# Optimization experiments

Hardware: AMD Instinct MI355X
Metric: run time of the kernel (lower is better)

## Reference

```python
import jax, jax.numpy as jnp
import numpy as np

IS_NORMAL = True
IS_SDF = False
WHITE_BACK = False


def setup_inputs() -> dict:
    key = jax.random.key(0)
    k1, k2, k3, k4 = jax.random.split(key, 4)
    B, R, S, C = 4, 16384, 64, 32
    colors = jax.random.uniform(k1, (B, R, S, C), dtype=jnp.float32)
    densities = jax.random.normal(k2, (B, R, S, 1), dtype=jnp.float32)
    depths = jax.random.uniform(k3, (B, R, S, 1), dtype=jnp.float32)
    grads = jax.random.normal(k4, (B, R, S, 3), dtype=jnp.float32)
    return {"colors": colors, "densities": densities, "depths": depths, "grads": grads}


def reference(colors, densities, depths, grads):
    # midpoint averaging along the sample axis (axis=2)
    deltas = depths[:, :, 1:] - depths[:, :, :-1]            # [B,R,S-1,1]
    colors_mid = (colors[:, :, :-1] + colors[:, :, 1:]) * 0.5
    densities_mid = (densities[:, :, :-1] + densities[:, :, 1:]) * 0.5
    depths_mid = (depths[:, :, :-1] + depths[:, :, 1:]) * 0.5
    grads_mid = (grads[:, :, :-1] + grads[:, :, 1:]) * 0.5

    if not IS_SDF:
        densities_mid = jax.nn.softplus(densities_mid - 1.0)

    density_delta = densities_mid * deltas
    alpha = 1.0 - jnp.exp(-density_delta)                     # [B,R,S-1,1]

    # transmittance via exclusive cumprod of (1 - alpha + 1e-10)
    alpha_shifted = jnp.concatenate(
        [jnp.ones_like(alpha[:, :, :1]), 1.0 - alpha + 1e-10], axis=2)
    weights = alpha * jnp.cumprod(alpha_shifted, axis=2)[:, :, :-1]

    composite_rgb = jnp.sum(weights * colors_mid, axis=2)     # [B,R,C]
    weight_total = jnp.sum(weights, axis=2)                   # [B,R,1]
    composite_depth = jnp.sum(weights * depths_mid, axis=2) / weight_total
    composite_depth = jnp.where(jnp.isnan(composite_depth), jnp.inf, composite_depth)
    composite_depth = jnp.clip(composite_depth, jnp.min(depths), jnp.max(depths))

    composite_grad = jnp.sum(weights * grads_mid, axis=2) + 1.0 - weight_total  # [B,R,3]

    if WHITE_BACK:
        composite_rgb = composite_rgb.at[..., :3].add(1.0 - weight_total)

    composite_rgb = composite_rgb * 2.0 - 1.0
    return (composite_rgb, composite_depth, weights, composite_grad)
```

## Files before the change

kernel.cpp:

```cpp
#include <hip/hip_runtime.h>
#include <math.h>

typedef float fvec4 __attribute__((ext_vector_type(4)));

template <int CTRL, int RM, int BM>
static __device__ __forceinline__ float updf(float oldv, float src) {
  return __int_as_float(__builtin_amdgcn_update_dpp(
      __float_as_int(oldv), __float_as_int(src), CTRL, RM, BM, false));
}

static __device__ __forceinline__ float mul_scan64(float x) {
  x *= updf<0x111, 0xf, 0xf>(1.0f, x);
  x *= updf<0x112, 0xf, 0xf>(1.0f, x);
  x *= updf<0x114, 0xf, 0xe>(1.0f, x);
  x *= updf<0x118, 0xf, 0xc>(1.0f, x);
  x *= updf<0x142, 0xa, 0xf>(1.0f, x);
  x *= updf<0x143, 0xc, 0xf>(1.0f, x);
  return x;
}
static __device__ __forceinline__ float sum64_lane63(float x) {
  x += updf<0x111, 0xf, 0xf>(0.0f, x);
  x += updf<0x112, 0xf, 0xf>(0.0f, x);
  x += updf<0x114, 0xf, 0xe>(0.0f, x);
  x += updf<0x118, 0xf, 0xc>(0.0f, x);
  x += updf<0x142, 0xa, 0xf>(0.0f, x);
  x += updf<0x143, 0xc, 0xf>(0.0f, x);
  return x;
}
static __device__ __forceinline__ float readlane63(float x) {
  return __int_as_float(__builtin_amdgcn_readlane(__float_as_int(x), 63));
}

__global__ __launch_bounds__(256) void minmax_kernel(const float4* __restrict__ d,
                                                     float* __restrict__ ws, int n4) {
  __shared__ float smin[4], smax[4];
  int idx = blockIdx.x * 256 + threadIdx.x;
  int stride = gridDim.x * 256;
  float lmin = INFINITY, lmax = -INFINITY;
  for (int i = idx; i < n4; i += stride) {
    float4 v = d[i];
    lmin = fminf(lmin, fminf(fminf(v.x, v.y), fminf(v.z, v.w)));
    lmax = fmaxf(lmax, fmaxf(fmaxf(v.x, v.y), fmaxf(v.z, v.w)));
  }
#pragma unroll
  for (int off = 32; off; off >>= 1) {
    lmin = fminf(lmin, __shfl_xor(lmin, off));
    lmax = fmaxf(lmax, __shfl_xor(lmax, off));
  }
  const int wid = threadIdx.x >> 6;
  if ((threadIdx.x & 63) == 0) { smin[wid] = lmin; smax[wid] = lmax; }
  __syncthreads();
  if (threadIdx.x == 0) {
    ws[blockIdx.x]       = fminf(fminf(smin[0], smin[1]), fminf(smin[2], smin[3]));
    ws[512 + blockIdx.x] = fmaxf(fmaxf(smax[0], smax[1]), fmaxf(smax[2], smax[3]));
  }
}

__global__ __launch_bounds__(256) void march_lite(
    const float* __restrict__ dens, const float* __restrict__ depths,
    const float* __restrict__ grads, float* __restrict__ out,
    float* __restrict__ coef_ws, const float* __restrict__ mm_part,
    size_t o_depth, size_t o_w, size_t o_grad)
{
  __shared__ float smin[4], smax[4];
  const int lane = threadIdx.x & 63;
  const int wid  = threadIdx.x >> 6;
  const size_t ray = (size_t)blockIdx.x * 4 + wid;

  const float d   = depths[ray * 64 + lane];
  const float den = __builtin_nontemporal_load(dens + ray * 64 + lane);
  const float* gp = grads + ray * 192 + (size_t)lane * 3;
  const float g0 = __builtin_nontemporal_load(gp + 0);
  const float g1 = __builtin_nontemporal_load(gp + 1);
  const float g2 = __builtin_nontemporal_load(gp + 2);

  const float dn    = __shfl_down(d, 1);
  const float denn  = __shfl_down(den, 1);
  const float delta = dn - d;
  const float dm    = 0.5f * (den + denn) - 1.0f;
  const float sp    = fmaxf(dm, 0.0f) + log1pf(expf(-fabsf(dm)));
  const float dd    = sp * delta;
  const float alpha = 1.0f - expf(-dd);
  const float t     = (1.0f - alpha) + 1e-10f;

  const float p = mul_scan64(t);
  float excl = __shfl_up(p, 1);
  if (lane == 0) excl = 1.0f;
  const float w = (lane < 63) ? alpha * excl : 0.0f;

  if (lane < 63)
    __builtin_nontemporal_store(w, out + o_w + ray * 63 + lane);

  float wprev = __shfl_up(w, 1);
  if (lane == 0) wprev = 0.0f;
  const float coef = 0.5f * (w + wprev);
  coef_ws[ray * 64 + lane] = coef;

  const float wt = readlane63(sum64_lane63(w));
  const float s1 = readlane63(sum64_lane63(coef * d));
  const float s2 = readlane63(sum64_lane63(coef * g0));
  const float s3 = readlane63(sum64_lane63(coef * g1));
  const float s4 = readlane63(sum64_lane63(coef * g2));

  {
    float m0 = fminf(mm_part[threadIdx.x], mm_part[threadIdx.x + 256]);
    float m1 = fmaxf(mm_part[512 + threadIdx.x], mm_part[512 + threadIdx.x + 256]);
#pragma unroll
    for (int off = 32; off; off >>= 1) {
      m0 = fminf(m0, __shfl_xor(m0, off));
      m1 = fmaxf(m1, __shfl_xor(m1, off));
    }
    if (lane == 0) { smin[wid] = m0; smax[wid] = m1; }
  }
  __syncthreads();

  if (lane == 0) {
    const float dmin = fminf(fminf(smin[0], smin[1]), fminf(smin[2], smin[3]));
    const float dmax = fmaxf(fmaxf(smax[0], smax[1]), fmaxf(smax[2], smax[3]));
    float cd = s1 / wt;
    if (cd != cd) cd = INFINITY;
    cd = fminf(fmaxf(cd, dmin), dmax);
    out[o_depth + ray] = cd;
    const float add = 1.0f - wt;
    float* og = out + o_grad + ray * 3;
    og[0] = s2 + add;
    og[1] = s3 + add;
    og[2] = s4 + add;
  }
}

__global__ __launch_bounds__(256) void rgb_kernel(
    const float* __restrict__ colors, const float* __restrict__ coef_ws,
    float* __restrict__ out)
{
  const int lane = threadIdx.x & 63;
  const size_t ray = (size_t)blockIdx.x * 4 + (threadIdx.x >> 6);

  const float coef = coef_ws[ray * 64 + lane];

  const fvec4* cp = (const fvec4*)(colors + ray * 2048);
  fvec4 col[8];
#pragma unroll
  for (int k = 0; k < 8; ++k)
    col[k] = __builtin_nontemporal_load(cp + (size_t)k * 64 + lane);

  float a0 = 0.f, a1 = 0.f, a2 = 0.f, a3 = 0.f;
  const int sbase = lane >> 3;
#pragma unroll
  for (int k = 0; k < 8; ++k) {
    const float cf = __shfl(coef, k * 8 + sbase);
    a0 = fmaf(cf, col[k].x, a0);
    a1 = fmaf(cf, col[k].y, a1);
    a2 = fmaf(cf, col[k].z, a2);
    a3 = fmaf(cf, col[k].w, a3);
  }
  a0 += updf<0x128, 0xf, 0xf>(0.0f, a0);
  a1 += updf<0x128, 0xf, 0xf>(0.0f, a1);
  a2 += updf<0x128, 0xf, 0xf>(0.0f, a2);
  a3 += updf<0x128, 0xf, 0xf>(0.0f, a3);
#pragma unroll
  for (int off = 16; off <= 32; off <<= 1) {
    a0 += __shfl_xor(a0, off);
    a1 += __shfl_xor(a1, off);
    a2 += __shfl_xor(a2, off);
    a3 += __shfl_xor(a3, off);
  }
  if (lane < 8) {
    float4 o;
    o.x = fmaf(a0, 2.0f, -1.0f);
    o.y = fmaf(a1, 2.0f, -1.0f);
    o.z = fmaf(a2, 2.0f, -1.0f);
    o.w = fmaf(a3, 2.0f, -1.0f);
    ((float4*)(out + ray * 32))[lane] = o;
  }
}

extern "C" void kernel_launch(void* const* d_in, const int* in_sizes, int n_in,
                              void* d_out, int out_size, void* d_ws, size_t ws_size,
                              hipStream_t stream) {
  const float* colors = (const float*)d_in[0];
  const float* dens   = (const float*)d_in[1];
  const float* depths = (const float*)d_in[2];
  const float* grads  = (const float*)d_in[3];
  float* out = (float*)d_out;
  float* ws  = (float*)d_ws;
  float* coef_ws = ws + 1024;

  const int ndep  = in_sizes[2];
  const int nrays = ndep / 64;
  const int C     = in_sizes[0] / ndep;

  const size_t o_depth = (size_t)nrays * C;
  const size_t o_w     = o_depth + (size_t)nrays;
  const size_t o_grad  = o_w + (size_t)nrays * 63;

  hipLaunchKernelGGL(minmax_kernel, dim3(512), dim3(256), 0, stream,
                     (const float4*)depths, ws, ndep / 4);
  hipLaunchKernelGGL(march_lite, dim3(nrays / 4), dim3(256), 0, stream,
                     dens, depths, grads, out, coef_ws, ws, o_depth, o_w, o_grad);
  hipLaunchKernelGGL(rgb_kernel, dim3(nrays / 4), dim3(256), 0, stream,
                     colors, coef_ws, out);
}
```

Baseline: 129.7 us.

## Fuse march and RGB kernels, fold depth min/max into main pass

Merges the march and RGB compositing kernels into one kernel where each wave processes four rays and keeps the blending coefficients in registers, removing the coef workspace round trip. The separate min/max pass over depths is removed; per-block min/max is computed from depths already loaded, then reduced by a single-block kernel, and a small final kernel applies the clamp to the stored unclamped depths. This avoids re-reading depths and the coef buffer, at the cost of two extra small launches, one of them a serial single-block reduction.

```diff
diff --git a/kernel.cpp b/kernel.cpp
--- a/kernel.cpp
+++ b/kernel.cpp
@@ -31,148 +31,155 @@
   return __int_as_float(__builtin_amdgcn_readlane(__float_as_int(x), 63));
 }
 
-__global__ __launch_bounds__(256) void minmax_kernel(const float4* __restrict__ d,
-                                                     float* __restrict__ ws, int n4) {
-  __shared__ float smin[4], smax[4];
-  int idx = blockIdx.x * 256 + threadIdx.x;
-  int stride = gridDim.x * 256;
-  float lmin = INFINITY, lmax = -INFINITY;
-  for (int i = idx; i < n4; i += stride) {
-    float4 v = d[i];
-    lmin = fminf(lmin, fminf(fminf(v.x, v.y), fminf(v.z, v.w)));
-    lmax = fmaxf(lmax, fmaxf(fmaxf(v.x, v.y), fmaxf(v.z, v.w)));
-  }
-#pragma unroll
-  for (int off = 32; off; off >>= 1) {
-    lmin = fminf(lmin, __shfl_xor(lmin, off));
-    lmax = fmaxf(lmax, __shfl_xor(lmax, off));
-  }
-  const int wid = threadIdx.x >> 6;
-  if ((threadIdx.x & 63) == 0) { smin[wid] = lmin; smax[wid] = lmax; }
-  __syncthreads();
-  if (threadIdx.x == 0) {
-    ws[blockIdx.x]       = fminf(fminf(smin[0], smin[1]), fminf(smin[2], smin[3]));
-    ws[512 + blockIdx.x] = fmaxf(fmaxf(smax[0], smax[1]), fmaxf(smax[2], smax[3]));
-  }
-}
-
-__global__ __launch_bounds__(256) void march_lite(
-    const float* __restrict__ dens, const float* __restrict__ depths,
-    const float* __restrict__ grads, float* __restrict__ out,
-    float* __restrict__ coef_ws, const float* __restrict__ mm_part,
-    size_t o_depth, size_t o_w, size_t o_grad)
+
+__global__ __launch_bounds__(256) void fused_kernel(
+    const float* __restrict__ colors, const float* __restrict__ dens,
+    const float* __restrict__ depths, const float* __restrict__ grads,
+    float* __restrict__ out, float* __restrict__ ws, float* __restrict__ cd_ws,
+    size_t o_w, size_t o_grad, int nb)
 {
   __shared__ float smin[4], smax[4];
   const int lane = threadIdx.x & 63;
   const int wid  = threadIdx.x >> 6;
-  const size_t ray = (size_t)blockIdx.x * 4 + wid;
-
-  const float d   = depths[ray * 64 + lane];
-  const float den = __builtin_nontemporal_load(dens + ray * 64 + lane);
-  const float* gp = grads + ray * 192 + (size_t)lane * 3;
-  const float g0 = __builtin_nontemporal_load(gp + 0);
-  const float g1 = __builtin_nontemporal_load(gp + 1);
-  const float g2 = __builtin_nontemporal_load(gp + 2);
-
-  const float dn    = __shfl_down(d, 1);
-  const float denn  = __shfl_down(den, 1);
-  const float delta = dn - d;
-  const float dm    = 0.5f * (den + denn) - 1.0f;
-  const float sp    = fmaxf(dm, 0.0f) + log1pf(expf(-fabsf(dm)));
-  const float dd    = sp * delta;
-  const float alpha = 1.0f - expf(-dd);
-  const float t     = (1.0f - alpha) + 1e-10f;
-
-  const float p = mul_scan64(t);
-  float excl = __shfl_up(p, 1);
-  if (lane == 0) excl = 1.0f;
-  const float w = (lane < 63) ? alpha * excl : 0.0f;
-
-  if (lane < 63)
-    __builtin_nontemporal_store(w, out + o_w + ray * 63 + lane);
-
-  float wprev = __shfl_up(w, 1);
-  if (lane == 0) wprev = 0.0f;
-  const float coef = 0.5f * (w + wprev);
-  coef_ws[ray * 64 + lane] = coef;
-
-  const float wt = readlane63(sum64_lane63(w));
-  const float s1 = readlane63(sum64_lane63(coef * d));
-  const float s2 = readlane63(sum64_lane63(coef * g0));
-  const float s3 = readlane63(sum64_lane63(coef * g1));
-  const float s4 = readlane63(sum64_lane63(coef * g2));
-
-  {
-    float m0 = fminf(mm_part[threadIdx.x], mm_part[threadIdx.x + 256]);
-    float m1 = fmaxf(mm_part[512 + threadIdx.x], mm_part[512 + threadIdx.x + 256]);
-#pragma unroll
-    for (int off = 32; off; off >>= 1) {
-      m0 = fminf(m0, __shfl_xor(m0, off));
-      m1 = fmaxf(m1, __shfl_xor(m1, off));
-    }
-    if (lane == 0) { smin[wid] = m0; smax[wid] = m1; }
-  }
+  const size_t ray0 = (size_t)blockIdx.x * 16 + (size_t)wid * 4;
+
+  float cf[4];
+  float dmin_w = INFINITY, dmax_w = -INFINITY;
+
+#pragma unroll
+  for (int r = 0; r < 4; ++r) {
+    const size_t ray = ray0 + r;
+    const float d   = depths[ray * 64 + lane];
+    const float den = __builtin_nontemporal_load(dens + ray * 64 + lane);
+    const float* gp = grads + ray * 192 + (size_t)lane * 3;
+    const float g0 = __builtin_nontemporal_load(gp + 0);
+    const float g1 = __builtin_nontemporal_load(gp + 1);
+    const float g2 = __builtin_nontemporal_load(gp + 2);
+
+    dmin_w = fminf(dmin_w, d);
+    dmax_w = fmaxf(dmax_w, d);
+
+    const float dn    = __shfl_down(d, 1);
+    const float denn  = __shfl_down(den, 1);
+    const float delta = dn - d;
+    const float dm    = 0.5f * (den + denn) - 1.0f;
+    const float sp    = fmaxf(dm, 0.0f) + log1pf(expf(-fabsf(dm)));
+    const float dd    = sp * delta;
+    const float alpha = 1.0f - expf(-dd);
+    const float t     = (1.0f - alpha) + 1e-10f;
+
+    const float p = mul_scan64(t);
+    float excl = __shfl_up(p, 1);
+    if (lane == 0) excl = 1.0f;
+    const float w = (lane < 63) ? alpha * excl : 0.0f;
+
+    if (lane < 63)
+      __builtin_nontemporal_store(w, out + o_w + ray * 63 + lane);
+
+    float wprev = __shfl_up(w, 1);
+    if (lane == 0) wprev = 0.0f;
+    const float coef = 0.5f * (w + wprev);
+    cf[r] = coef;
+
+    const float wt = readlane63(sum64_lane63(w));
+    const float s1 = readlane63(sum64_lane63(coef * d));
+    const float s2 = readlane63(sum64_lane63(coef * g0));
+    const float s3 = readlane63(sum64_lane63(coef * g1));
+    const float s4 = readlane63(sum64_lane63(coef * g2));
+
+    if (lane == 0) {
+      float cd = s1 / wt;
+      if (cd != cd) cd = INFINITY;
+      cd_ws[ray] = cd;
+      const float add = 1.0f - wt;
+      float* og = out + o_grad + ray * 3;
+      og[0] = s2 + add;
+      og[1] = s3 + add;
+      og[2] = s4 + add;
+    }
+  }
+
+#pragma unroll
+  for (int off = 32; off; off >>= 1) {
+    dmin_w = fminf(dmin_w, __shfl_xor(dmin_w, off));
+    dmax_w = fmaxf(dmax_w, __shfl_xor(dmax_w, off));
+  }
+  if (lane == 0) { smin[wid] = dmin_w; smax[wid] = dmax_w; }
   __syncthreads();
-
-  if (lane == 0) {
-    const float dmin = fminf(fminf(smin[0], smin[1]), fminf(smin[2], smin[3]));
-    const float dmax = fmaxf(fmaxf(smax[0], smax[1]), fmaxf(smax[2], smax[3]));
-    float cd = s1 / wt;
-    if (cd != cd) cd = INFINITY;
-    cd = fminf(fmaxf(cd, dmin), dmax);
-    out[o_depth + ray] = cd;
-    const float add = 1.0f - wt;
-    float* og = out + o_grad + ray * 3;
-    og[0] = s2 + add;
-    og[1] = s3 + add;
-    og[2] = s4 + add;
-  }
-}
-
-__global__ __launch_bounds__(256) void rgb_kernel(
-    const float* __restrict__ colors, const float* __restrict__ coef_ws,
-    float* __restrict__ out)
+  if (threadIdx.x == 0) {
+    ws[blockIdx.x]      = fminf(fminf(smin[0], smin[1]), fminf(smin[2], smin[3]));
+    ws[nb + blockIdx.x] = fmaxf(fmaxf(smax[0], smax[1]), fmaxf(smax[2], smax[3]));
+  }
+
+  const int sbase = lane >> 3;
+#pragma unroll
+  for (int r = 0; r < 4; ++r) {
+    const size_t ray = ray0 + r;
+    const fvec4* cp = (const fvec4*)(colors + ray * 2048);
+    fvec4 col[8];
+#pragma unroll
+    for (int k = 0; k < 8; ++k)
+      col[k] = __builtin_nontemporal_load(cp + (size_t)k * 64 + lane);
+
+    float a0 = 0.f, a1 = 0.f, a2 = 0.f, a3 = 0.f;
+#pragma unroll
+    for (int k = 0; k < 8; ++k) {
+      const float cfb = __shfl(cf[r], k * 8 + sbase);
+      a0 = fmaf(cfb, col[k].x, a0);
+      a1 = fmaf(cfb, col[k].y, a1);
+      a2 = fmaf(cfb, col[k].z, a2);
+      a3 = fmaf(cfb, col[k].w, a3);
+    }
+    a0 += updf<0x128, 0xf, 0xf>(0.0f, a0);
+    a1 += updf<0x128, 0xf, 0xf>(0.0f, a1);
+    a2 += updf<0x128, 0xf, 0xf>(0.0f, a2);
+    a3 += updf<0x128, 0xf, 0xf>(0.0f, a3);
+#pragma unroll
+    for (int off = 16; off <= 32; off <<= 1) {
+      a0 += __shfl_xor(a0, off);
+      a1 += __shfl_xor(a1, off);
+      a2 += __shfl_xor(a2, off);
+      a3 += __shfl_xor(a3, off);
+    }
+    if (lane < 8) {
+      float4 o;
+      o.x = fmaf(a0, 2.0f, -1.0f);
+      o.y = fmaf(a1, 2.0f, -1.0f);
+      o.z = fmaf(a2, 2.0f, -1.0f);
+      o.w = fmaf(a3, 2.0f, -1.0f);
+      ((float4*)(out + ray * 32))[lane] = o;
+    }
+  }
+}
+
+__global__ __launch_bounds__(256) void reduce_kernel(float* __restrict__ ws, int nb) {
+  __shared__ float smin[4], smax[4];
+  float m0 = INFINITY, m1 = -INFINITY;
+  for (int j = threadIdx.x; j < nb; j += 256) {
+    m0 = fminf(m0, ws[j]);
+    m1 = fmaxf(m1, ws[nb + j]);
+  }
+#pragma unroll
+  for (int off = 32; off; off >>= 1) {
+    m0 = fminf(m0, __shfl_xor(m0, off));
+    m1 = fmaxf(m1, __shfl_xor(m1, off));
+  }
+  const int wid = threadIdx.x >> 6;
+  if ((threadIdx.x & 63) == 0) { smin[wid] = m0; smax[wid] = m1; }
+  __syncthreads();
+  if (threadIdx.x == 0) {
+    ws[2 * nb]     = fminf(fminf(smin[0], smin[1]), fminf(smin[2], smin[3]));
+    ws[2 * nb + 1] = fmaxf(fmaxf(smax[0], smax[1]), fmaxf(smax[2], smax[3]));
+  }
+}
+
+__global__ __launch_bounds__(256) void depth_kernel(
+    const float* __restrict__ cd_ws, const float* __restrict__ mm,
+    float* __restrict__ out, size_t o_depth)
 {
-  const int lane = threadIdx.x & 63;
-  const size_t ray = (size_t)blockIdx.x * 4 + (threadIdx.x >> 6);
-
-  const float coef = coef_ws[ray * 64 + lane];
-
-  const fvec4* cp = (const fvec4*)(colors + ray * 2048);
-  fvec4 col[8];
-#pragma unroll
-  for (int k = 0; k < 8; ++k)
-    col[k] = __builtin_nontemporal_load(cp + (size_t)k * 64 + lane);
-
-  float a0 = 0.f, a1 = 0.f, a2 = 0.f, a3 = 0.f;
-  const int sbase = lane >> 3;
-#pragma unroll
-  for (int k = 0; k < 8; ++k) {
-    const float cf = __shfl(coef, k * 8 + sbase);
-    a0 = fmaf(cf, col[k].x, a0);
-    a1 = fmaf(cf, col[k].y, a1);
-    a2 = fmaf(cf, col[k].z, a2);
-    a3 = fmaf(cf, col[k].w, a3);
-  }
-  a0 += updf<0x128, 0xf, 0xf>(0.0f, a0);
-  a1 += updf<0x128, 0xf, 0xf>(0.0f, a1);
-  a2 += updf<0x128, 0xf, 0xf>(0.0f, a2);
-  a3 += updf<0x128, 0xf, 0xf>(0.0f, a3);
-#pragma unroll
-  for (int off = 16; off <= 32; off <<= 1) {
-    a0 += __shfl_xor(a0, off);
-    a1 += __shfl_xor(a1, off);
-    a2 += __shfl_xor(a2, off);
-    a3 += __shfl_xor(a3, off);
-  }
-  if (lane < 8) {
-    float4 o;
-    o.x = fmaf(a0, 2.0f, -1.0f);
-    o.y = fmaf(a1, 2.0f, -1.0f);
-    o.z = fmaf(a2, 2.0f, -1.0f);
-    o.w = fmaf(a3, 2.0f, -1.0f);
-    ((float4*)(out + ray * 32))[lane] = o;
-  }
+  const int i = blockIdx.x * 256 + threadIdx.x;
+  const float dmin = mm[0], dmax = mm[1];
+  out[o_depth + i] = fminf(fmaxf(cd_ws[i], dmin), dmax);
 }
 
 extern "C" void kernel_launch(void* const* d_in, const int* in_sizes, int n_in,
@@ -184,7 +191,6 @@
   const float* grads  = (const float*)d_in[3];
   float* out = (float*)d_out;
   float* ws  = (float*)d_ws;
-  float* coef_ws = ws + 1024;
 
   const int ndep  = in_sizes[2];
   const int nrays = ndep / 64;
@@ -194,10 +200,12 @@
   const size_t o_w     = o_depth + (size_t)nrays;
   const size_t o_grad  = o_w + (size_t)nrays * 63;
 
-  hipLaunchKernelGGL(minmax_kernel, dim3(512), dim3(256), 0, stream,
-                     (const float4*)depths, ws, ndep / 4);
-  hipLaunchKernelGGL(march_lite, dim3(nrays / 4), dim3(256), 0, stream,
-                     dens, depths, grads, out, coef_ws, ws, o_depth, o_w, o_grad);
-  hipLaunchKernelGGL(rgb_kernel, dim3(nrays / 4), dim3(256), 0, stream,
-                     colors, coef_ws, out);
-}
+  const int nb = nrays / 16;
+  float* cd_ws = ws + 2 * (size_t)nb + 64;
+
+  hipLaunchKernelGGL(fused_kernel, dim3(nb), dim3(256), 0, stream,
+                     colors, dens, depths, grads, out, ws, cd_ws, o_w, o_grad, nb);
+  hipLaunchKernelGGL(reduce_kernel, dim3(1), dim3(256), 0, stream, ws, nb);
+  hipLaunchKernelGGL(depth_kernel, dim3(nrays / 256), dim3(256), 0, stream,
+                     cd_ws, ws + 2 * (size_t)nb, out, o_depth);
+}
```

Result: faster. 125.8 us (-3.0%).

## Fuse march and RGB kernels, processing four rays per wavefront

Applied to the files above, without the earlier changes.

Merges the weight/depth/grad kernel and the color compositing kernel into one launch, so per-sample coefficients stay in registers instead of going through a workspace buffer. Each wavefront now handles four rays, which spreads the per-block min/max partial reduction over more work. The cost is a grid a quarter of the size and more live registers, which may reduce occupancy and latency hiding on the large colors stream.

```diff
diff --git a/kernel.cpp b/kernel.cpp
--- a/kernel.cpp
+++ b/kernel.cpp
@@ -30,6 +30,7 @@
 static __device__ __forceinline__ float readlane63(float x) {
   return __int_as_float(__builtin_amdgcn_readlane(__float_as_int(x), 63));
 }
+
 
 __global__ __launch_bounds__(256) void minmax_kernel(const float4* __restrict__ d,
                                                      float* __restrict__ ws, int n4) {
@@ -56,51 +57,16 @@
   }
 }
 
-__global__ __launch_bounds__(256) void march_lite(
-    const float* __restrict__ dens, const float* __restrict__ depths,
-    const float* __restrict__ grads, float* __restrict__ out,
-    float* __restrict__ coef_ws, const float* __restrict__ mm_part,
+__global__ __launch_bounds__(256) void fused_kernel(
+    const float* __restrict__ colors, const float* __restrict__ dens,
+    const float* __restrict__ depths, const float* __restrict__ grads,
+    float* __restrict__ out, const float* __restrict__ mm_part,
     size_t o_depth, size_t o_w, size_t o_grad)
 {
   __shared__ float smin[4], smax[4];
   const int lane = threadIdx.x & 63;
   const int wid  = threadIdx.x >> 6;
-  const size_t ray = (size_t)blockIdx.x * 4 + wid;
-
-  const float d   = depths[ray * 64 + lane];
-  const float den = __builtin_nontemporal_load(dens + ray * 64 + lane);
-  const float* gp = grads + ray * 192 + (size_t)lane * 3;
-  const float g0 = __builtin_nontemporal_load(gp + 0);
-  const float g1 = __builtin_nontemporal_load(gp + 1);
-  const float g2 = __builtin_nontemporal_load(gp + 2);
-
-  const float dn    = __shfl_down(d, 1);
-  const float denn  = __shfl_down(den, 1);
-  const float delta = dn - d;
-  const float dm    = 0.5f * (den + denn) - 1.0f;
-  const float sp    = fmaxf(dm, 0.0f) + log1pf(expf(-fabsf(dm)));
-  const float dd    = sp * delta;
-  const float alpha = 1.0f - expf(-dd);
-  const float t     = (1.0f - alpha) + 1e-10f;
-
-  const float p = mul_scan64(t);
-  float excl = __shfl_up(p, 1);
-  if (lane == 0) excl = 1.0f;
-  const float w = (lane < 63) ? alpha * excl : 0.0f;
-
-  if (lane < 63)
-    __builtin_nontemporal_store(w, out + o_w + ray * 63 + lane);
-
-  float wprev = __shfl_up(w, 1);
-  if (lane == 0) wprev = 0.0f;
-  const float coef = 0.5f * (w + wprev);
-  coef_ws[ray * 64 + lane] = coef;
-
-  const float wt = readlane63(sum64_lane63(w));
-  const float s1 = readlane63(sum64_lane63(coef * d));
-  const float s2 = readlane63(sum64_lane63(coef * g0));
-  const float s3 = readlane63(sum64_lane63(coef * g1));
-  const float s4 = readlane63(sum64_lane63(coef * g2));
+  const size_t ray0 = (size_t)blockIdx.x * 16 + (size_t)wid * 4;
 
   {
     float m0 = fminf(mm_part[threadIdx.x], mm_part[threadIdx.x + 256]);
@@ -113,65 +79,99 @@
     if (lane == 0) { smin[wid] = m0; smax[wid] = m1; }
   }
   __syncthreads();
-
-  if (lane == 0) {
-    const float dmin = fminf(fminf(smin[0], smin[1]), fminf(smin[2], smin[3]));
-    const float dmax = fmaxf(fmaxf(smax[0], smax[1]), fmaxf(smax[2], smax[3]));
-    float cd = s1 / wt;
-    if (cd != cd) cd = INFINITY;
-    cd = fminf(fmaxf(cd, dmin), dmax);
-    out[o_depth + ray] = cd;
-    const float add = 1.0f - wt;
-    float* og = out + o_grad + ray * 3;
-    og[0] = s2 + add;
-    og[1] = s3 + add;
-    og[2] = s4 + add;
-  }
-}
-
-__global__ __launch_bounds__(256) void rgb_kernel(
-    const float* __restrict__ colors, const float* __restrict__ coef_ws,
-    float* __restrict__ out)
-{
-  const int lane = threadIdx.x & 63;
-  const size_t ray = (size_t)blockIdx.x * 4 + (threadIdx.x >> 6);
-
-  const float coef = coef_ws[ray * 64 + lane];
-
-  const fvec4* cp = (const fvec4*)(colors + ray * 2048);
-  fvec4 col[8];
-#pragma unroll
-  for (int k = 0; k < 8; ++k)
-    col[k] = __builtin_nontemporal_load(cp + (size_t)k * 64 + lane);
-
-  float a0 = 0.f, a1 = 0.f, a2 = 0.f, a3 = 0.f;
+  const float dmin = fminf(fminf(smin[0], smin[1]), fminf(smin[2], smin[3]));
+  const float dmax = fmaxf(fmaxf(smax[0], smax[1]), fmaxf(smax[2], smax[3]));
+
+  float cf[4];
+
+#pragma unroll
+  for (int r = 0; r < 4; ++r) {
+    const size_t ray = ray0 + r;
+    const float d   = depths[ray * 64 + lane];
+    const float den = __builtin_nontemporal_load(dens + ray * 64 + lane);
+    const float* gp = grads + ray * 192 + (size_t)lane * 3;
+    const float g0 = __builtin_nontemporal_load(gp + 0);
+    const float g1 = __builtin_nontemporal_load(gp + 1);
+    const float g2 = __builtin_nontemporal_load(gp + 2);
+
+    const float dn    = __shfl_down(d, 1);
+    const float denn  = __shfl_down(den, 1);
+    const float delta = dn - d;
+    const float dm    = 0.5f * (den + denn) - 1.0f;
+    const float sp    = fmaxf(dm, 0.0f) + log1pf(expf(-fabsf(dm)));
+    const float dd    = sp * delta;
+    const float alpha = 1.0f - expf(-dd);
+    const float t     = (1.0f - alpha) + 1e-10f;
+
+    const float p = mul_scan64(t);
+    float excl = __shfl_up(p, 1);
+    if (lane == 0) excl = 1.0f;
+    const float w = (lane < 63) ? alpha * excl : 0.0f;
+
+    if (lane < 63)
+      __builtin_nontemporal_store(w, out + o_w + ray * 63 + lane);
+
+    float wprev = __shfl_up(w, 1);
+    if (lane == 0) wprev = 0.0f;
+    const float coef = 0.5f * (w + wprev);
+    cf[r] = coef;
+
+    const float wt = readlane63(sum64_lane63(w));
+    const float s1 = readlane63(sum64_lane63(coef * d));
+    const float s2 = readlane63(sum64_lane63(coef * g0));
+    const float s3 = readlane63(sum64_lane63(coef * g1));
+    const float s4 = readlane63(sum64_lane63(coef * g2));
+
+    if (lane == 0) {
+      float cd = s1 / wt;
+      if (cd != cd) cd = INFINITY;
+      out[o_depth + ray] = fminf(fmaxf(cd, dmin), dmax);
+      const float add = 1.0f - wt;
+      float* og = out + o_grad + ray * 3;
+      og[0] = s2 + add;
+      og[1] = s3 + add;
+      og[2] = s4 + add;
+    }
+  }
+
   const int sbase = lane >> 3;
 #pragma unroll
-  for (int k = 0; k < 8; ++k) {
-    const float cf = __shfl(coef, k * 8 + sbase);
-    a0 = fmaf(cf, col[k].x, a0);
-    a1 = fmaf(cf, col[k].y, a1);
-    a2 = fmaf(cf, col[k].z, a2);
-    a3 = fmaf(cf, col[k].w, a3);
-  }
-  a0 += updf<0x128, 0xf, 0xf>(0.0f, a0);
-  a1 += updf<0x128, 0xf, 0xf>(0.0f, a1);
-  a2 += updf<0x128, 0xf, 0xf>(0.0f, a2);
-  a3 += updf<0x128, 0xf, 0xf>(0.0f, a3);
-#pragma unroll
-  for (int off = 16; off <= 32; off <<= 1) {
-    a0 += __shfl_xor(a0, off);
-    a1 += __shfl_xor(a1, off);
-    a2 += __shfl_xor(a2, off);
-    a3 += __shfl_xor(a3, off);
-  }
-  if (lane < 8) {
-    float4 o;
-    o.x = fmaf(a0, 2.0f, -1.0f);
-    o.y = fmaf(a1, 2.0f, -1.0f);
-    o.z = fmaf(a2, 2.0f, -1.0f);
-    o.w = fmaf(a3, 2.0f, -1.0f);
-    ((float4*)(out + ray * 32))[lane] = o;
+  for (int r = 0; r < 4; ++r) {
+    const size_t ray = ray0 + r;
+    const fvec4* cp = (const fvec4*)(colors + ray * 2048);
+    fvec4 col[8];
+#pragma unroll
+    for (int k = 0; k < 8; ++k)
+      col[k] = __builtin_nontemporal_load(cp + (size_t)k * 64 + lane);
+
+    float a0 = 0.f, a1 = 0.f, a2 = 0.f, a3 = 0.f;
+#pragma unroll
+    for (int k = 0; k < 8; ++k) {
+      const float cfb = __shfl(cf[r], k * 8 + sbase);
+      a0 = fmaf(cfb, col[k].x, a0);
+      a1 = fmaf(cfb, col[k].y, a1);
+      a2 = fmaf(cfb, col[k].z, a2);
+      a3 = fmaf(cfb, col[k].w, a3);
+    }
+    a0 += updf<0x128, 0xf, 0xf>(0.0f, a0);
+    a1 += updf<0x128, 0xf, 0xf>(0.0f, a1);
+    a2 += updf<0x128, 0xf, 0xf>(0.0f, a2);
+    a3 += updf<0x128, 0xf, 0xf>(0.0f, a3);
+#pragma unroll
+    for (int off = 16; off <= 32; off <<= 1) {
+      a0 += __shfl_xor(a0, off);
+      a1 += __shfl_xor(a1, off);
+      a2 += __shfl_xor(a2, off);
+      a3 += __shfl_xor(a3, off);
+    }
+    if (lane < 8) {
+      float4 o;
+      o.x = fmaf(a0, 2.0f, -1.0f);
+      o.y = fmaf(a1, 2.0f, -1.0f);
+      o.z = fmaf(a2, 2.0f, -1.0f);
+      o.w = fmaf(a3, 2.0f, -1.0f);
+      ((float4*)(out + ray * 32))[lane] = o;
+    }
   }
 }
 
@@ -184,7 +184,6 @@
   const float* grads  = (const float*)d_in[3];
   float* out = (float*)d_out;
   float* ws  = (float*)d_ws;
-  float* coef_ws = ws + 1024;
 
   const int ndep  = in_sizes[2];
   const int nrays = ndep / 64;
@@ -196,8 +195,6 @@
 
   hipLaunchKernelGGL(minmax_kernel, dim3(512), dim3(256), 0, stream,
                      (const float4*)depths, ws, ndep / 4);
-  hipLaunchKernelGGL(march_lite, dim3(nrays / 4), dim3(256), 0, stream,
-                     dens, depths, grads, out, coef_ws, ws, o_depth, o_w, o_grad);
-  hipLaunchKernelGGL(rgb_kernel, dim3(nrays / 4), dim3(256), 0, stream,
-                     colors, coef_ws, out);
-}
+  hipLaunchKernelGGL(fused_kernel, dim3(nrays / 16), dim3(256), 0, stream,
+                     colors, dens, depths, grads, out, ws, o_depth, o_w, o_grad);
+}
```

Measured after the change: 123.7 us, median of 2. 4.6% less time.
